# Kernel optimization log

Hardware: AMD Instinct MI355X
Metric: run time of the kernel (lower is better)

The kernel has to match this reference:

```python
import jax, jax.numpy as jnp
import numpy as np

B, N, D = 8, 2048, 512  # batch, input_dim (tokens), weight_dim


def setup_inputs() -> dict:
    key = jax.random.key(0)
    ks = jax.random.split(key, 7)
    return {
        "query": jax.random.normal(ks[0], (B, N, D), dtype=jnp.float32),
        "key": jax.random.normal(ks[1], (B, N, D), dtype=jnp.float32),
        "value": jax.random.normal(ks[2], (B, N, D), dtype=jnp.float32),
        "W_query": jax.random.normal(ks[3], (D, D), dtype=jnp.float32),
        "W_key": jax.random.normal(ks[4], (D, D), dtype=jnp.float32),
        "W_value": jax.random.normal(ks[5], (D, D), dtype=jnp.float32),
        "self_importance": jnp.zeros((N,), dtype=jnp.float32),
    }


def reference(query, key, value, W_query, W_key, W_value, self_importance):
    d = W_query.shape[0]
    q = jnp.einsum("bnd,de->bne", query, W_query)
    k = jnp.einsum("bnd,de->bne", key, W_key)
    v = jnp.einsum("bnd,de->bne", value, W_value)
    scores = jnp.einsum("bqe,bke->bqk", q, k) / jnp.sqrt(jnp.float32(d))
    # diagonal self-importance bias: eye(N) * clamp(exp(s), max=3)
    importance = jnp.minimum(jnp.exp(self_importance), 3.0)  # [N]
    n = scores.shape[1]
    idx = jnp.arange(n)
    scores = scores.at[:, idx, idx].add(importance)
    attn = jax.nn.softmax(scores, axis=-1)  # [B, N, N]
    entropy_loss = -jnp.mean(jnp.sum(attn * jnp.log(attn + 1e-10), axis=-1))
    out = jnp.einsum("bqk,bke->bqe", attn, v)
    return (out, attn, entropy_loss)
```

## Files before the change

kernel.cpp:

```cpp
#include <hip/hip_runtime.h>
#include <math.h>

#define BB 8
#define NN 2048
#define DD 512

typedef _Float16 halfT;
typedef _Float16 half8 __attribute__((ext_vector_type(8)));
typedef _Float16 half4 __attribute__((ext_vector_type(4)));
typedef float f32x4 __attribute__((ext_vector_type(4)));

#define GLOAD16(gp, sp) __builtin_amdgcn_global_load_lds( \
    (const __attribute__((address_space(1))) void*)(gp), \
    (__attribute__((address_space(3))) void*)(sp), 16, 0, 0)

__global__ __launch_bounds__(256) void wsplit_kernel(
    const float* __restrict__ Wq, const float* __restrict__ Wk, const float* __restrict__ Wv,
    _Float16* __restrict__ qhT, _Float16* __restrict__ qlT,
    _Float16* __restrict__ khT, _Float16* __restrict__ klT,
    _Float16* __restrict__ vhT)
{
    __shared__ float t[64][65];
    const int z = blockIdx.z;
    const float* W = (z == 0) ? Wq : ((z == 1) ? Wk : Wv);
    _Float16* Ph = (z == 0) ? qhT : ((z == 1) ? khT : vhT);
    _Float16* Pl = (z == 0) ? qlT : ((z == 1) ? klT : nullptr);
    const int bx = blockIdx.x * 64, by = blockIdx.y * 64;
    const int tid = threadIdx.x;
    #pragma unroll
    for (int i = 0; i < 16; ++i) {
        const int idx = i * 256 + tid;
        const int r = idx >> 6, c = idx & 63;
        t[r][c] = W[(long)(by + r) * 512 + bx + c];
    }
    __syncthreads();
    #pragma unroll
    for (int i = 0; i < 16; ++i) {
        const int idx = i * 256 + tid;
        const int r = idx >> 6, c = idx & 63;
        const float v = t[c][r];
        const _Float16 h = (_Float16)v;
        const long o = (long)(bx + r) * 512 + by + c;
        Ph[o] = h;
        if (z < 2) Pl[o] = (_Float16)(v - (float)h);
    }
}

template<int EPI>
__global__ __launch_bounds__(256) void mm_nt(
    const float* __restrict__ Af,
    const _Float16* __restrict__ Agh, const _Float16* __restrict__ Agl,
    const _Float16* __restrict__ Bgh, const _Float16* __restrict__ Bgl,
    float* __restrict__ Of, _Float16* __restrict__ Oh, _Float16* __restrict__ Ol,
    const float* __restrict__ si,
    int N, int K, long sAb, long sBb, long sOb, float scale)
{
    constexpr bool NP3    = (EPI == 0);
    constexpr bool A_FP32 = (EPI == 0 || EPI == 1);
    constexpr bool A_SPLIT = (EPI == 0);

    __shared__ __align__(16) _Float16 smem[(NP3 ? 4 : 2) * 128 * 32];
    _Float16* Ah = smem;
    _Float16* Bh = smem + 4096;
    _Float16* Al = smem + 8192;
    _Float16* Bl = smem + 12288;

    const int tid  = threadIdx.x;
    const int lane = tid & 63;
    const int w    = tid >> 6;
    const int wr   = w >> 1, wc = w & 1;
    const int z    = blockIdx.z;
    const int bm   = blockIdx.y * 128, bn = blockIdx.x * 128;

    const float* Afz = nullptr;
    const _Float16 *Aghz = nullptr, *Aglz = nullptr;
    if constexpr (A_FP32) { Afz = Af + (long)z * sAb; }
    else { Aghz = Agh + (long)z * sAb; if constexpr (NP3) Aglz = Agl + (long)z * sAb; }
    const _Float16* Bghz = Bgh + (long)z * sBb;
    const _Float16* Bglz = nullptr;
    if constexpr (NP3) Bglz = Bgl + (long)z * sBb;

    f32x4 acc[4][4];
    #pragma unroll
    for (int i = 0; i < 4; ++i)
        #pragma unroll
        for (int j = 0; j < 4; ++j) acc[i][j] = (f32x4)0.0f;

    for (int k0 = 0; k0 < K; k0 += 32) {
        #pragma unroll
        for (int i = 0; i < 2; ++i) {
            const int c   = i * 256 + w * 64 + lane;
            const int row = c >> 2, sl = c & 3;
            const long g  = (long)(bn + row) * K + k0 + sl * 8;
            const int lb  = (i * 256 + w * 64) * 8;
            GLOAD16(Bghz + g, Bh + lb);
            if constexpr (NP3) GLOAD16(Bglz + g, Bl + lb);
        }
        if constexpr (A_FP32) {
            #pragma unroll
            for (int i = 0; i < 4; ++i) {
                const int c = tid + i * 256;
                const int row = c >> 3, q4 = c & 7;
                const float4 v = *(const float4*)(Afz + (long)(bm + row) * K + k0 + q4 * 4);
                half4 h;
                h[0] = (_Float16)v.x; h[1] = (_Float16)v.y;
                h[2] = (_Float16)v.z; h[3] = (_Float16)v.w;
                *(half4*)&Ah[row * 32 + q4 * 4] = h;
                if constexpr (A_SPLIT) {
                    half4 l;
                    l[0] = (_Float16)(v.x - (float)h[0]);
                    l[1] = (_Float16)(v.y - (float)h[1]);
                    l[2] = (_Float16)(v.z - (float)h[2]);
                    l[3] = (_Float16)(v.w - (float)h[3]);
                    *(half4*)&Al[row * 32 + q4 * 4] = l;
                }
            }
        } else {
            #pragma unroll
            for (int i = 0; i < 2; ++i) {
                const int c   = i * 256 + w * 64 + lane;
                const int row = c >> 2, sl = c & 3;
                const long g  = (long)(bm + row) * K + k0 + sl * 8;
                const int lb  = (i * 256 + w * 64) * 8;
                GLOAD16(Aghz + g, Ah + lb);
            }
        }
        __syncthreads();

        half8 ah[4], bh[4], al[4], bl[4];
        #pragma unroll
        for (int f = 0; f < 4; ++f) {
            const int ar = wr * 64 + f * 16 + (lane & 15);
            const int ao = ar * 32 + ((lane >> 4) << 3);
            ah[f] = *(const half8*)&Ah[ao];
            if constexpr (NP3) al[f] = *(const half8*)&Al[ao];
            const int br = wc * 64 + f * 16 + (lane & 15);
            const int bo = br * 32 + ((lane >> 4) << 3);
            bh[f] = *(const half8*)&Bh[bo];
            if constexpr (NP3) bl[f] = *(const half8*)&Bl[bo];
        }
        #pragma unroll
        for (int i = 0; i < 4; ++i)
            #pragma unroll
            for (int j = 0; j < 4; ++j) {
                acc[i][j] = __builtin_amdgcn_mfma_f32_16x16x32_f16(ah[i], bh[j], acc[i][j], 0, 0, 0);
                if constexpr (NP3) {
                    acc[i][j] = __builtin_amdgcn_mfma_f32_16x16x32_f16(ah[i], bl[j], acc[i][j], 0, 0, 0);
                    acc[i][j] = __builtin_amdgcn_mfma_f32_16x16x32_f16(al[i], bh[j], acc[i][j], 0, 0, 0);
                }
            }
        __syncthreads();
    }

    #pragma unroll
    for (int i = 0; i < 4; ++i) {
        const int rb = bm + wr * 64 + i * 16 + ((lane >> 4) << 2);
        #pragma unroll
        for (int j = 0; j < 4; ++j) {
            const int gc = bn + wc * 64 + j * 16 + (lane & 15);
            if constexpr (EPI == 0) {
                #pragma unroll
                for (int r = 0; r < 4; ++r) {
                    const float vv = acc[i][j][r];
                    const _Float16 h = (_Float16)vv;
                    const long o = (long)(rb + r) * N + gc;
                    Oh[o] = h;
                    Ol[o] = (_Float16)(vv - (float)h);
                }
            } else if constexpr (EPI == 1) {
                half4 hv;
                #pragma unroll
                for (int r = 0; r < 4; ++r) hv[r] = (_Float16)acc[i][j][r];
                const int b = rb >> 11, rIn = rb & 2047;
                *(half4*)&Oh[((long)b * 512 + gc) * 2048 + rIn] = hv;
            } else {
                float* O = Of + (long)z * sOb;
                #pragma unroll
                for (int r = 0; r < 4; ++r)
                    O[(long)(rb + r) * N + gc] = acc[i][j][r];
            }
        }
    }
}

__global__ __launch_bounds__(512, 2) void scores256_kernel(
    const halfT* __restrict__ qh, const halfT* __restrict__ ql,
    const halfT* __restrict__ kh, const halfT* __restrict__ kl,
    float* __restrict__ C, const float* __restrict__ si, float scale)
{
    extern __shared__ __align__(16) char smem[];

    const int tid  = threadIdx.x;
    const int lane = tid & 63;
    const int w    = tid >> 6;
    const int wr   = w >> 2, wc = w & 3;

    int flat = (blockIdx.z << 6) | (blockIdx.y << 3) | blockIdx.x;
    flat = ((flat & 7) << 6) | (flat >> 3);
    const int bx = flat & 7, by = (flat >> 3) & 7, bz = flat >> 6;
    const int bm = by * 256, bn = bx * 256;

    const long zoff = (long)bz * NN * DD;
    const halfT* A_h = qh + zoff;
    const halfT* A_l = ql + zoff;
    const halfT* B_h = kh + zoff;
    const halfT* B_l = kl + zoff;

    const int s_row   = w * 16 + (lane >> 2);
    const int s_chunk = (lane & 3) ^ ((lane >> 3) & 3);
    const long gA = (long)(bm + s_row) * DD + s_chunk * 8;
    const long gB = (long)(bn + s_row) * DD + s_chunk * 8;

    auto stage = [&](char* buf, int t) {
        const long kk = (long)t * 32;
        #pragma unroll
        for (int i = 0; i < 2; ++i) {
            const long ra = gA + (long)i * 128 * DD + kk;
            const long rb = gB + (long)i * 128 * DD + kk;
            char* d = buf + i * 8192 + w * 1024;
            GLOAD16(A_h + ra, d);
            GLOAD16(A_l + ra, d + 16384);
            GLOAD16(B_h + rb, d + 32768);
            GLOAD16(B_l + rb, d + 49152);
        }
    };

    const int lr   = lane & 15;
    const int q16  = lane >> 4;
    const int fswz = (lr >> 1) & 3;
    const int frag = lr * 64 + ((q16 ^ fswz) << 4);
    const int abase = wr * 8192 + frag;
    const int bbase = wc * 4096 + frag;

    f32x4 acc[8][4];
    #pragma unroll
    for (int m = 0; m < 8; ++m)
        #pragma unroll
        for (int n = 0; n < 4; ++n) acc[m][n] = (f32x4)0.0f;

    stage(smem, 0);
    asm volatile("s_waitcnt vmcnt(0)" ::: "memory");
    __builtin_amdgcn_s_barrier();

    for (int t = 0; t < 16; ++t) {
        char* cur = smem + (size_t)(t & 1) * 65536;
        char* nxt = smem + (size_t)((t + 1) & 1) * 65536;

        if (t < 15) stage(nxt, t + 1);

        half8 ah[8], bh[4], bl[4];
        #pragma unroll
        for (int n = 0; n < 4; ++n)
            bh[n] = *(const half8*)(cur + 32768 + bbase + n * 1024);
        #pragma unroll
        for (int m = 0; m < 8; ++m)
            ah[m] = *(const half8*)(cur + abase + m * 1024);
        __builtin_amdgcn_s_setprio(1);
        #pragma unroll
        for (int m = 0; m < 8; ++m)
            #pragma unroll
            for (int n = 0; n < 4; ++n)
                acc[m][n] = __builtin_amdgcn_mfma_f32_16x16x32_f16(ah[m], bh[n], acc[m][n], 0, 0, 0);
        __builtin_amdgcn_s_setprio(0);

        #pragma unroll
        for (int n = 0; n < 4; ++n)
            bl[n] = *(const half8*)(cur + 49152 + bbase + n * 1024);
        __builtin_amdgcn_s_setprio(1);
        #pragma unroll
        for (int m = 0; m < 8; ++m)
            #pragma unroll
            for (int n = 0; n < 4; ++n)
                acc[m][n] = __builtin_amdgcn_mfma_f32_16x16x32_f16(ah[m], bl[n], acc[m][n], 0, 0, 0);
        __builtin_amdgcn_s_setprio(0);

        __builtin_amdgcn_s_setprio(1);
        #pragma unroll
        for (int m = 0; m < 8; ++m) {
            const half8 al = *(const half8*)(cur + 16384 + abase + m * 1024);
            #pragma unroll
            for (int n = 0; n < 4; ++n)
                acc[m][n] = __builtin_amdgcn_mfma_f32_16x16x32_f16(al, bh[n], acc[m][n], 0, 0, 0);
        }
        __builtin_amdgcn_s_setprio(0);

        if (t < 15) {
            asm volatile("s_waitcnt vmcnt(0)" ::: "memory");
            __builtin_amdgcn_s_barrier();
        }
    }

    float* Cz = C + (long)bz * NN * NN;
    #pragma unroll
    for (int m = 0; m < 8; ++m) {
        const int rb = bm + wr * 128 + m * 16 + ((lane >> 4) << 2);
        #pragma unroll
        for (int n = 0; n < 4; ++n) {
            const int gc = bn + wc * 64 + n * 16 + (lane & 15);
            #pragma unroll
            for (int r = 0; r < 4; ++r) {
                const int gr = rb + r;
                float vv = acc[m][n][r] * scale;
                if (gr == gc) vv += fminf(expf(si[gr]), 3.0f);
                Cz[(long)gr * NN + gc] = vv;
            }
        }
    }
}

__global__ __launch_bounds__(256) void softmax_entropy_kernel(
    float* __restrict__ attn, _Float16* __restrict__ ah, float* __restrict__ partials)
{
    __shared__ float red[4];
    const long row = blockIdx.x;
    float* p = attn + row * (long)NN;
    _Float16* ph = ah + row * (long)NN;
    const int tid = threadIdx.x;
    const int base = tid * 8;

    float4 va = *(const float4*)(p + base);
    float4 vb = *(const float4*)(p + base + 4);
    float v[8] = {va.x, va.y, va.z, va.w, vb.x, vb.y, vb.z, vb.w};

    float m = v[0];
    #pragma unroll
    for (int i = 1; i < 8; ++i) m = fmaxf(m, v[i]);
    #pragma unroll
    for (int o = 32; o; o >>= 1) m = fmaxf(m, __shfl_xor(m, o, 64));
    if ((tid & 63) == 0) red[tid >> 6] = m;
    __syncthreads();
    m = fmaxf(fmaxf(red[0], red[1]), fmaxf(red[2], red[3]));

    float t[8];
    float s = 0.f;
    #pragma unroll
    for (int i = 0; i < 8; ++i) { t[i] = v[i] - m; v[i] = expf(t[i]); s += v[i]; }
    #pragma unroll
    for (int o = 32; o; o >>= 1) s += __shfl_xor(s, o, 64);
    __syncthreads();
    if ((tid & 63) == 0) red[tid >> 6] = s;
    __syncthreads();
    s = red[0] + red[1] + red[2] + red[3];

    const float inv = 1.0f / s;
    const float lns = logf(s);
    float e = 0.f;
    float pv[8];
    #pragma unroll
    for (int i = 0; i < 8; ++i) {
        pv[i] = v[i] * inv;
        e = fmaf(pv[i], t[i] - lns, e);
    }
    *(float4*)(p + base)     = make_float4(pv[0], pv[1], pv[2], pv[3]);
    *(float4*)(p + base + 4) = make_float4(pv[4], pv[5], pv[6], pv[7]);
    half8 h;
    #pragma unroll
    for (int i = 0; i < 8; ++i) h[i] = (_Float16)pv[i];
    *(half8*)(ph + base) = h;

    #pragma unroll
    for (int o = 32; o; o >>= 1) e += __shfl_xor(e, o, 64);
    __syncthreads();
    if ((tid & 63) == 0) red[tid >> 6] = e;
    __syncthreads();
    if (tid == 0) partials[row] = red[0] + red[1] + red[2] + red[3];
}

__global__ __launch_bounds__(256) void ent_reduce_kernel(
    const float* __restrict__ partials, float* __restrict__ ent)
{
    __shared__ float red[4];
    float s = 0.f;
    for (int i = threadIdx.x; i < BB * NN; i += 256) s += partials[i];
    #pragma unroll
    for (int o = 32; o; o >>= 1) s += __shfl_xor(s, o, 64);
    if ((threadIdx.x & 63) == 0) red[threadIdx.x >> 6] = s;
    __syncthreads();
    if (threadIdx.x == 0)
        *ent = -(red[0] + red[1] + red[2] + red[3]) / (float)(BB * NN);
}

extern "C" void kernel_launch(void* const* d_in, const int* in_sizes, int n_in,
                              void* d_out, int out_size, void* d_ws, size_t ws_size,
                              hipStream_t stream) {
    const float* query = (const float*)d_in[0];
    const float* key   = (const float*)d_in[1];
    const float* value = (const float*)d_in[2];
    const float* Wq    = (const float*)d_in[3];
    const float* Wk    = (const float*)d_in[4];
    const float* Wv    = (const float*)d_in[5];
    const float* si    = (const float*)d_in[6];

    float* out  = (float*)d_out;
    float* attn = out + (size_t)BB * NN * DD;
    float* ent  = attn + (size_t)BB * NN * NN;

    const size_t NK = (size_t)BB * NN * DD;
    _Float16* ws16 = (_Float16*)d_ws;
    _Float16* qh = ws16;
    _Float16* ql = qh + NK;
    _Float16* kh = ql + NK;
    _Float16* kl = kh + NK;
    _Float16* vT = kl + NK;
    _Float16* WqhT = vT + NK;
    _Float16* WqlT = WqhT + DD * DD;
    _Float16* WkhT = WqlT + DD * DD;
    _Float16* WklT = WkhT + DD * DD;
    _Float16* WvhT = WklT + DD * DD;
    float* partials = (float*)(WvhT + DD * DD);
    _Float16* attn_h = ws16;

    const dim3 blk(256);
    const float inv_sqrt_d = 0.044194173824159216f;

    wsplit_kernel<<<dim3(8, 8, 3), blk, 0, stream>>>(Wq, Wk, Wv,
        WqhT, WqlT, WkhT, WklT, WvhT);

    mm_nt<0><<<dim3(4, 128, 1), blk, 0, stream>>>(
        query, nullptr, nullptr, WqhT, WqlT, nullptr, qh, ql, nullptr,
        DD, DD, 0, 0, 0, 1.0f);
    mm_nt<0><<<dim3(4, 128, 1), blk, 0, stream>>>(
        key, nullptr, nullptr, WkhT, WklT, nullptr, kh, kl, nullptr,
        DD, DD, 0, 0, 0, 1.0f);
    mm_nt<1><<<dim3(4, 128, 1), blk, 0, stream>>>(
        value, nullptr, nullptr, WvhT, nullptr, nullptr, vT, nullptr, nullptr,
        DD, DD, 0, 0, 0, 1.0f);

    scores256_kernel<<<dim3(8, 8, 8), dim3(512), 131072, stream>>>(
        qh, ql, kh, kl, attn, si, inv_sqrt_d);

    softmax_entropy_kernel<<<dim3(BB * NN), blk, 0, stream>>>(attn, attn_h, partials);
    ent_reduce_kernel<<<dim3(1), blk, 0, stream>>>(partials, ent);

    mm_nt<3><<<dim3(4, 16, BB), blk, 0, stream>>>(
        nullptr, attn_h, nullptr, vT, nullptr, out, nullptr, nullptr, nullptr,
        DD, NN, (long)NN * NN, (long)DD * NN, (long)NN * DD, 1.0f);
}
```

Before: 336.5 us.

## Deepen scores-kernel prefetch to two stages and merge Q/K projection launches

The scores kernel switches from whole-tile double buffering to per-unit staging, where each of the four hi/lo A/B sub-tiles is reloaded for step t+2 right after its last LDS read, under finer barriers and partial vmcnt waits. This aims to overlap more global-to-LDS traffic with MFMA work and hide load latency. The Q and K split-precision projections also merge into one launch with a z dimension of two, cutting a launch and filling the GPU better. The extra barriers per iteration add sync overhead, and the hand-tuned vmcnt counts risk subtle ordering bugs.

```diff
diff --git a/kernel.cpp b/kernel.cpp
--- a/kernel.cpp
+++ b/kernel.cpp
@@ -46,24 +46,120 @@
     }
 }
 
-template<int EPI>
-__global__ __launch_bounds__(256) void mm_nt(
-    const float* __restrict__ Af,
-    const _Float16* __restrict__ Agh, const _Float16* __restrict__ Agl,
-    const _Float16* __restrict__ Bgh, const _Float16* __restrict__ Bgl,
-    float* __restrict__ Of, _Float16* __restrict__ Oh, _Float16* __restrict__ Ol,
-    const float* __restrict__ si,
-    int N, int K, long sAb, long sBb, long sOb, float scale)
+__global__ __launch_bounds__(256) void projqk_kernel(
+    const float* __restrict__ Af0, const float* __restrict__ Af1,
+    const _Float16* __restrict__ B0h, const _Float16* __restrict__ B0l,
+    const _Float16* __restrict__ B1h, const _Float16* __restrict__ B1l,
+    _Float16* __restrict__ O0h, _Float16* __restrict__ O0l,
+    _Float16* __restrict__ O1h, _Float16* __restrict__ O1l)
 {
-    constexpr bool NP3    = (EPI == 0);
-    constexpr bool A_FP32 = (EPI == 0 || EPI == 1);
-    constexpr bool A_SPLIT = (EPI == 0);
-
-    __shared__ __align__(16) _Float16 smem[(NP3 ? 4 : 2) * 128 * 32];
+    __shared__ __align__(16) _Float16 smem[4 * 128 * 32];
     _Float16* Ah = smem;
     _Float16* Bh = smem + 4096;
     _Float16* Al = smem + 8192;
     _Float16* Bl = smem + 12288;
+
+    const int z = blockIdx.z;
+    const float* Af = z ? Af1 : Af0;
+    const _Float16* Bgh = z ? B1h : B0h;
+    const _Float16* Bgl = z ? B1l : B0l;
+    _Float16* Oh = z ? O1h : O0h;
+    _Float16* Ol = z ? O1l : O0l;
+
+    const int tid  = threadIdx.x;
+    const int lane = tid & 63;
+    const int w    = tid >> 6;
+    const int wr   = w >> 1, wc = w & 1;
+    const int bm   = blockIdx.y * 128, bn = blockIdx.x * 128;
+
+    f32x4 acc[4][4];
+    #pragma unroll
+    for (int i = 0; i < 4; ++i)
+        #pragma unroll
+        for (int j = 0; j < 4; ++j) acc[i][j] = (f32x4)0.0f;
+
+    for (int k0 = 0; k0 < DD; k0 += 32) {
+        #pragma unroll
+        for (int i = 0; i < 2; ++i) {
+            const int c   = i * 256 + w * 64 + lane;
+            const int row = c >> 2, sl = c & 3;
+            const long g  = (long)(bn + row) * DD + k0 + sl * 8;
+            const int lb  = (i * 256 + w * 64) * 8;
+            GLOAD16(Bgh + g, Bh + lb);
+            GLOAD16(Bgl + g, Bl + lb);
+        }
+        #pragma unroll
+        for (int i = 0; i < 4; ++i) {
+            const int c = tid + i * 256;
+            const int row = c >> 3, q4 = c & 7;
+            const float4 v = *(const float4*)(Af + (long)(bm + row) * DD + k0 + q4 * 4);
+            half4 h;
+            h[0] = (_Float16)v.x; h[1] = (_Float16)v.y;
+            h[2] = (_Float16)v.z; h[3] = (_Float16)v.w;
+            *(half4*)&Ah[row * 32 + q4 * 4] = h;
+            half4 l;
+            l[0] = (_Float16)(v.x - (float)h[0]);
+            l[1] = (_Float16)(v.y - (float)h[1]);
+            l[2] = (_Float16)(v.z - (float)h[2]);
+            l[3] = (_Float16)(v.w - (float)h[3]);
+            *(half4*)&Al[row * 32 + q4 * 4] = l;
+        }
+        __syncthreads();
+
+        half8 ah[4], bh[4], al[4], bl[4];
+        #pragma unroll
+        for (int f = 0; f < 4; ++f) {
+            const int ar = wr * 64 + f * 16 + (lane & 15);
+            const int ao = ar * 32 + ((lane >> 4) << 3);
+            ah[f] = *(const half8*)&Ah[ao];
+            al[f] = *(const half8*)&Al[ao];
+            const int br = wc * 64 + f * 16 + (lane & 15);
+            const int bo = br * 32 + ((lane >> 4) << 3);
+            bh[f] = *(const half8*)&Bh[bo];
+            bl[f] = *(const half8*)&Bl[bo];
+        }
+        #pragma unroll
+        for (int i = 0; i < 4; ++i)
+            #pragma unroll
+            for (int j = 0; j < 4; ++j) {
+                acc[i][j] = __builtin_amdgcn_mfma_f32_16x16x32_f16(ah[i], bh[j], acc[i][j], 0, 0, 0);
+                acc[i][j] = __builtin_amdgcn_mfma_f32_16x16x32_f16(ah[i], bl[j], acc[i][j], 0, 0, 0);
+                acc[i][j] = __builtin_amdgcn_mfma_f32_16x16x32_f16(al[i], bh[j], acc[i][j], 0, 0, 0);
+            }
+        __syncthreads();
+    }
+
+    #pragma unroll
+    for (int i = 0; i < 4; ++i) {
+        const int rb = bm + wr * 64 + i * 16 + ((lane >> 4) << 2);
+        #pragma unroll
+        for (int j = 0; j < 4; ++j) {
+            const int gc = bn + wc * 64 + j * 16 + (lane & 15);
+            #pragma unroll
+            for (int r = 0; r < 4; ++r) {
+                const float vv = acc[i][j][r];
+                const _Float16 h = (_Float16)vv;
+                const long o = (long)(rb + r) * DD + gc;
+                Oh[o] = h;
+                Ol[o] = (_Float16)(vv - (float)h);
+            }
+        }
+    }
+}
+
+template<int EPI>
+__global__ __launch_bounds__(256) void mm_nt(
+    const float* __restrict__ Af,
+    const _Float16* __restrict__ Agh,
+    const _Float16* __restrict__ Bgh,
+    float* __restrict__ Of, _Float16* __restrict__ Oh,
+    int N, int K, long sAb, long sBb, long sOb)
+{
+    constexpr bool A_FP32 = (EPI == 1);
+
+    __shared__ __align__(16) _Float16 smem[2 * 128 * 32];
+    _Float16* Ah = smem;
+    _Float16* Bh = smem + 4096;
 
     const int tid  = threadIdx.x;
     const int lane = tid & 63;
@@ -73,12 +169,10 @@
     const int bm   = blockIdx.y * 128, bn = blockIdx.x * 128;
 
     const float* Afz = nullptr;
-    const _Float16 *Aghz = nullptr, *Aglz = nullptr;
+    const _Float16* Aghz = nullptr;
     if constexpr (A_FP32) { Afz = Af + (long)z * sAb; }
-    else { Aghz = Agh + (long)z * sAb; if constexpr (NP3) Aglz = Agl + (long)z * sAb; }
+    else { Aghz = Agh + (long)z * sAb; }
     const _Float16* Bghz = Bgh + (long)z * sBb;
-    const _Float16* Bglz = nullptr;
-    if constexpr (NP3) Bglz = Bgl + (long)z * sBb;
 
     f32x4 acc[4][4];
     #pragma unroll
@@ -94,7 +188,6 @@
             const long g  = (long)(bn + row) * K + k0 + sl * 8;
             const int lb  = (i * 256 + w * 64) * 8;
             GLOAD16(Bghz + g, Bh + lb);
-            if constexpr (NP3) GLOAD16(Bglz + g, Bl + lb);
         }
         if constexpr (A_FP32) {
             #pragma unroll
@@ -106,14 +199,6 @@
                 h[0] = (_Float16)v.x; h[1] = (_Float16)v.y;
                 h[2] = (_Float16)v.z; h[3] = (_Float16)v.w;
                 *(half4*)&Ah[row * 32 + q4 * 4] = h;
-                if constexpr (A_SPLIT) {
-                    half4 l;
-                    l[0] = (_Float16)(v.x - (float)h[0]);
-                    l[1] = (_Float16)(v.y - (float)h[1]);
-                    l[2] = (_Float16)(v.z - (float)h[2]);
-                    l[3] = (_Float16)(v.w - (float)h[3]);
-                    *(half4*)&Al[row * 32 + q4 * 4] = l;
-                }
             }
         } else {
             #pragma unroll
@@ -127,28 +212,21 @@
         }
         __syncthreads();
 
-        half8 ah[4], bh[4], al[4], bl[4];
+        half8 ah[4], bh[4];
         #pragma unroll
         for (int f = 0; f < 4; ++f) {
             const int ar = wr * 64 + f * 16 + (lane & 15);
             const int ao = ar * 32 + ((lane >> 4) << 3);
             ah[f] = *(const half8*)&Ah[ao];
-            if constexpr (NP3) al[f] = *(const half8*)&Al[ao];
             const int br = wc * 64 + f * 16 + (lane & 15);
             const int bo = br * 32 + ((lane >> 4) << 3);
             bh[f] = *(const half8*)&Bh[bo];
-            if constexpr (NP3) bl[f] = *(const half8*)&Bl[bo];
         }
         #pragma unroll
         for (int i = 0; i < 4; ++i)
             #pragma unroll
-            for (int j = 0; j < 4; ++j) {
+            for (int j = 0; j < 4; ++j)
                 acc[i][j] = __builtin_amdgcn_mfma_f32_16x16x32_f16(ah[i], bh[j], acc[i][j], 0, 0, 0);
-                if constexpr (NP3) {
-                    acc[i][j] = __builtin_amdgcn_mfma_f32_16x16x32_f16(ah[i], bl[j], acc[i][j], 0, 0, 0);
-                    acc[i][j] = __builtin_amdgcn_mfma_f32_16x16x32_f16(al[i], bh[j], acc[i][j], 0, 0, 0);
-                }
-            }
         __syncthreads();
     }
 
@@ -158,16 +236,7 @@
         #pragma unroll
         for (int j = 0; j < 4; ++j) {
             const int gc = bn + wc * 64 + j * 16 + (lane & 15);
-            if constexpr (EPI == 0) {
-                #pragma unroll
-                for (int r = 0; r < 4; ++r) {
-                    const float vv = acc[i][j][r];
-                    const _Float16 h = (_Float16)vv;
-                    const long o = (long)(rb + r) * N + gc;
-                    Oh[o] = h;
-                    Ol[o] = (_Float16)(vv - (float)h);
-                }
-            } else if constexpr (EPI == 1) {
+            if constexpr (EPI == 1) {
                 half4 hv;
                 #pragma unroll
                 for (int r = 0; r < 4; ++r) hv[r] = (_Float16)acc[i][j][r];
@@ -210,25 +279,17 @@
     const int s_chunk = (lane & 3) ^ ((lane >> 3) & 3);
     const long gA = (long)(bm + s_row) * DD + s_chunk * 8;
     const long gB = (long)(bn + s_row) * DD + s_chunk * 8;
-
-    auto stage = [&](char* buf, int t) {
-        const long kk = (long)t * 32;
-        #pragma unroll
-        for (int i = 0; i < 2; ++i) {
-            const long ra = gA + (long)i * 128 * DD + kk;
-            const long rb = gB + (long)i * 128 * DD + kk;
-            char* d = buf + i * 8192 + w * 1024;
-            GLOAD16(A_h + ra, d);
-            GLOAD16(A_l + ra, d + 16384);
-            GLOAD16(B_h + rb, d + 32768);
-            GLOAD16(B_l + rb, d + 49152);
-        }
-    };
+    const int ldst = w * 1024;
+
+#define STAGE_UNIT(P, G, T, S) do { \
+        const long _kk = (long)(T) * 32; \
+        GLOAD16((P) + (G) + _kk,                  smem + (S) * 16384 + ldst); \
+        GLOAD16((P) + (G) + (long)128 * DD + _kk, smem + (S) * 16384 + 8192 + ldst); \
+    } while (0)
 
     const int lr   = lane & 15;
     const int q16  = lane >> 4;
-    const int fswz = (lr >> 1) & 3;
-    const int frag = lr * 64 + ((q16 ^ fswz) << 4);
+    const int frag = lr * 64 + ((q16 ^ ((lr >> 1) & 3)) << 4);
     const int abase = wr * 8192 + frag;
     const int bbase = wc * 4096 + frag;
 
@@ -238,23 +299,34 @@
         #pragma unroll
         for (int n = 0; n < 4; ++n) acc[m][n] = (f32x4)0.0f;
 
-    stage(smem, 0);
-    asm volatile("s_waitcnt vmcnt(0)" ::: "memory");
+    STAGE_UNIT(A_h, gA, 0, 0); STAGE_UNIT(A_l, gA, 0, 1);
+    STAGE_UNIT(B_h, gB, 0, 2); STAGE_UNIT(B_l, gB, 0, 3);
+    STAGE_UNIT(A_h, gA, 1, 4); STAGE_UNIT(A_l, gA, 1, 5);
+    STAGE_UNIT(B_h, gB, 1, 6); STAGE_UNIT(B_l, gB, 1, 7);
+    asm volatile("s_waitcnt vmcnt(8)" ::: "memory");
     __builtin_amdgcn_s_barrier();
+    __builtin_amdgcn_sched_barrier(0);
 
     for (int t = 0; t < 16; ++t) {
-        char* cur = smem + (size_t)(t & 1) * 65536;
-        char* nxt = smem + (size_t)((t + 1) & 1) * 65536;
-
-        if (t < 15) stage(nxt, t + 1);
+        const int base = (t & 1) * 4;
+        const char* uAh = smem + (size_t)(base + 0) * 16384;
+        const char* uAl = smem + (size_t)(base + 1) * 16384;
+        const char* uBh = smem + (size_t)(base + 2) * 16384;
+        const char* uBl = smem + (size_t)(base + 3) * 16384;
+        const bool pf = (t < 14);
 
         half8 ah[8], bh[4], bl[4];
         #pragma unroll
         for (int n = 0; n < 4; ++n)
-            bh[n] = *(const half8*)(cur + 32768 + bbase + n * 1024);
+            bh[n] = *(const half8*)(uBh + bbase + n * 1024);
         #pragma unroll
         for (int m = 0; m < 8; ++m)
-            ah[m] = *(const half8*)(cur + abase + m * 1024);
+            ah[m] = *(const half8*)(uAh + abase + m * 1024);
+        asm volatile("s_waitcnt lgkmcnt(0)" ::: "memory");
+        __builtin_amdgcn_sched_barrier(0);
+        __builtin_amdgcn_s_barrier();
+        __builtin_amdgcn_sched_barrier(0);
+        if (pf) { STAGE_UNIT(A_h, gA, t + 2, base + 0); STAGE_UNIT(B_h, gB, t + 2, base + 2); }
         __builtin_amdgcn_s_setprio(1);
         #pragma unroll
         for (int m = 0; m < 8; ++m)
@@ -265,7 +337,12 @@
 
         #pragma unroll
         for (int n = 0; n < 4; ++n)
-            bl[n] = *(const half8*)(cur + 49152 + bbase + n * 1024);
+            bl[n] = *(const half8*)(uBl + bbase + n * 1024);
+        asm volatile("s_waitcnt lgkmcnt(0)" ::: "memory");
+        __builtin_amdgcn_sched_barrier(0);
+        __builtin_amdgcn_s_barrier();
+        __builtin_amdgcn_sched_barrier(0);
+        if (pf) STAGE_UNIT(B_l, gB, t + 2, base + 3);
         __builtin_amdgcn_s_setprio(1);
         #pragma unroll
         for (int m = 0; m < 8; ++m)
@@ -274,21 +351,31 @@
                 acc[m][n] = __builtin_amdgcn_mfma_f32_16x16x32_f16(ah[m], bl[n], acc[m][n], 0, 0, 0);
         __builtin_amdgcn_s_setprio(0);
 
+        half8 al[8];
+        #pragma unroll
+        for (int m = 0; m < 8; ++m)
+            al[m] = *(const half8*)(uAl + abase + m * 1024);
+        asm volatile("s_waitcnt lgkmcnt(0)" ::: "memory");
+        __builtin_amdgcn_sched_barrier(0);
+        __builtin_amdgcn_s_barrier();
+        __builtin_amdgcn_sched_barrier(0);
+        if (pf) STAGE_UNIT(A_l, gA, t + 2, base + 1);
         __builtin_amdgcn_s_setprio(1);
         #pragma unroll
-        for (int m = 0; m < 8; ++m) {
-            const half8 al = *(const half8*)(cur + 16384 + abase + m * 1024);
+        for (int m = 0; m < 8; ++m)
             #pragma unroll
             for (int n = 0; n < 4; ++n)
-                acc[m][n] = __builtin_amdgcn_mfma_f32_16x16x32_f16(al, bh[n], acc[m][n], 0, 0, 0);
-        }
+                acc[m][n] = __builtin_amdgcn_mfma_f32_16x16x32_f16(al[m], bh[n], acc[m][n], 0, 0, 0);
         __builtin_amdgcn_s_setprio(0);
 
         if (t < 15) {
-            asm volatile("s_waitcnt vmcnt(0)" ::: "memory");
+            if (t < 14) { asm volatile("s_waitcnt vmcnt(8)" ::: "memory"); }
+            else        { asm volatile("s_waitcnt vmcnt(0)" ::: "memory"); }
             __builtin_amdgcn_s_barrier();
-        }
-    }
+            __builtin_amdgcn_sched_barrier(0);
+        }
+    }
+#undef STAGE_UNIT
 
     float* Cz = C + (long)bz * NN * NN;
     #pragma unroll
@@ -416,15 +503,10 @@
     wsplit_kernel<<<dim3(8, 8, 3), blk, 0, stream>>>(Wq, Wk, Wv,
         WqhT, WqlT, WkhT, WklT, WvhT);
 
-    mm_nt<0><<<dim3(4, 128, 1), blk, 0, stream>>>(
-        query, nullptr, nullptr, WqhT, WqlT, nullptr, qh, ql, nullptr,
-        DD, DD, 0, 0, 0, 1.0f);
-    mm_nt<0><<<dim3(4, 128, 1), blk, 0, stream>>>(
-        key, nullptr, nullptr, WkhT, WklT, nullptr, kh, kl, nullptr,
-        DD, DD, 0, 0, 0, 1.0f);
+    projqk_kernel<<<dim3(4, 128, 2), blk, 0, stream>>>(
+        query, key, WqhT, WqlT, WkhT, WklT, qh, ql, kh, kl);
     mm_nt<1><<<dim3(4, 128, 1), blk, 0, stream>>>(
-        value, nullptr, nullptr, WvhT, nullptr, nullptr, vT, nullptr, nullptr,
-        DD, DD, 0, 0, 0, 1.0f);
+        value, nullptr, WvhT, nullptr, vT, DD, DD, 0, 0, 0);
 
     scores256_kernel<<<dim3(8, 8, 8), dim3(512), 131072, stream>>>(
         qh, ql, kh, kl, attn, si, inv_sqrt_d);
@@ -433,6 +515,6 @@
     ent_reduce_kernel<<<dim3(1), blk, 0, stream>>>(partials, ent);
 
     mm_nt<3><<<dim3(4, 16, BB), blk, 0, stream>>>(
-        nullptr, attn_h, nullptr, vT, nullptr, out, nullptr, nullptr, nullptr,
-        DD, NN, (long)NN * NN, (long)DD * NN, (long)NN * DD, 1.0f);
-}
+        nullptr, attn_h, vT, out, nullptr, DD, NN,
+        (long)NN * NN, (long)DD * NN, (long)NN * DD);
+}
```

After: 336.7 us. Within noise of the previous version (+0.1%).
